# Optimization experiments

Hardware: AMD Instinct MI355X
Metric: run time of the kernel (lower is better)

The kernel has to match this reference:

```python
import jax, jax.numpy as jnp
import numpy as np

# PiGNNLayer(d_emb=128, n_heads=1, n_neighbors=30); N nodes, E = N*K edges, BSZ graphs
N, K, H, D = 16384, 30, 1, 128
E = N * K
DH = D // H  # d_head
BSZ = 1      # batch_idx is all zeros (see notes: gating broadcast requires bsz==1)


def setup_inputs() -> dict:
    key = jax.random.key(0)
    ks = jax.random.split(key, 16)

    def W(k, i, o):
        return jax.random.normal(k, (i, o), jnp.float32) / np.float32(np.sqrt(i))

    inp = {
        "h": jax.random.normal(ks[0], (N, D), jnp.float32),
        "e": jax.random.normal(ks[1], (E, D), jnp.float32),
        # att_mlp: Linear(3D,D) ReLU Linear(D,D) ReLU Linear(D,H)
        "aw1": W(ks[2], 3 * D, D), "ab1": jnp.zeros((D,), jnp.float32),
        "aw2": W(ks[3], D, D),     "ab2": jnp.zeros((D,), jnp.float32),
        "aw3": W(ks[4], D, H),     "ab3": jnp.zeros((H,), jnp.float32),
        # node_mlp: Linear(2D,D) GELU Linear(D,D) GELU Linear(D,D)
        "nw1": W(ks[5], 2 * D, D), "nb1": jnp.zeros((D,), jnp.float32),
        "nw2": W(ks[6], D, D),     "nb2": jnp.zeros((D,), jnp.float32),
        "nw3": W(ks[7], D, D),     "nb3": jnp.zeros((D,), jnp.float32),
        # to_h: Linear(D, D, bias=False)
        "thw": W(ks[8], H * D, D),
        # gate_mlp: Linear(D,D) ReLU Linear(D,D) ReLU Linear(D,D)
        "gw1": W(ks[9], D, D),  "gb1": jnp.zeros((D,), jnp.float32),
        "gw2": W(ks[10], D, D), "gb2": jnp.zeros((D,), jnp.float32),
        "gw3": W(ks[11], D, D), "gb3": jnp.zeros((D,), jnp.float32),
        # edge_idx[0] = source node i repeated K times (required by '(i j)' reshape)
        "edge_idx": jnp.stack([
            jnp.repeat(jnp.arange(N, dtype=jnp.int32), K),
            jax.random.randint(ks[12], (E,), 0, N, dtype=jnp.int32),
        ]),
        "batch_idx": jnp.zeros((N,), jnp.int32),
    }
    return inp


def reference(h, e, aw1, ab1, aw2, ab2, aw3, ab3,
              nw1, nb1, nw2, nb2, nw3, nb3, thw,
              gw1, gb1, gw2, gb2, gw3, gb3,
              edge_idx, batch_idx):
    src, dst = edge_idx[0], edge_idx[1]
    hi, hj = h[src], h[dst]                       # [E, D] gathers
    cat3 = jnp.concatenate([hi, e, hj], axis=-1)  # [E, 3D]
    cat2 = jnp.concatenate([e, hj], axis=-1)      # [E, 2D]

    # attention logits per head, grouped (i j) -> [H, N, K]
    w = jax.nn.relu(cat3 @ aw1 + ab1)
    w = jax.nn.relu(w @ aw2 + ab2)
    w = (w @ aw3 + ab3)                           # [E, H]
    w = jnp.transpose(w.reshape(N, K, H), (2, 0, 1)) / jnp.sqrt(jnp.float32(DH))
    att = jax.nn.softmax(w, axis=-1)              # softmax over neighbors j

    # values per edge (exact GELU, matching torch nn.GELU default)
    v = jax.nn.gelu(cat2 @ nw1 + nb1, approximate=False)
    v = jax.nn.gelu(v @ nw2 + nb2, approximate=False)
    v = (v @ nw3 + nb3).reshape(N, K, D)          # [N, K, D]

    hh = jnp.einsum('hij,ijd->ihd', att, v).reshape(N, H * D)  # 'h i d -> i (h d)'
    hh = hh @ thw                                 # to_h (no bias)

    # scatter_mean over batch (segment-sum form of the dense-mask trick)
    csum = jax.ops.segment_sum(hh, batch_idx, num_segments=BSZ)
    cnt = jax.ops.segment_sum(jnp.ones((N, 1), hh.dtype), batch_idx, num_segments=BSZ)
    c = csum / cnt                                # [BSZ, D]

    g = jax.nn.relu(c @ gw1 + gb1)
    g = jax.nn.relu(g @ gw2 + gb2)
    g = jax.nn.sigmoid(g @ gw3 + gb3)             # [BSZ, D]
    return hh * g[batch_idx]                      # per-node gate gather
```

## Files before the change

### kernel.cpp

```cpp
#include <hip/hip_runtime.h>
#include <math.h>

#define NN 16384
#define KNB 30
#define NE (NN*KNB)

typedef __attribute__((ext_vector_type(8))) __bf16 bf16x8;
typedef __attribute__((ext_vector_type(4))) float f32x4;
typedef unsigned short ushortT;
typedef __attribute__((ext_vector_type(8))) unsigned short ushort8v;

#define SWZ(r) (((r)&7)<<4)

__device__ __forceinline__ ushortT f2bf(float x){
  __bf16 b = (__bf16)x;
  union { __bf16 b; ushortT u; } v; v.b = b; return v.u;
}
__device__ __forceinline__ float bf2f(ushortT u){
  union { unsigned int u32; float f; } v; v.u32 = ((unsigned int)u) << 16;
  return v.f;
}
__device__ __forceinline__ float bf2f_lo(unsigned int w){
  union { unsigned int u32; float f; } v; v.u32 = w << 16; return v.f;
}
__device__ __forceinline__ float bf2f_hi(unsigned int w){
  union { unsigned int u32; float f; } v; v.u32 = w & 0xffff0000u; return v.f;
}
__device__ __forceinline__ float gelu_f(float x){
  float ax = fabsf(x) * 0.7071067811865476f;
  float t = 1.0f / (1.0f + 0.47047f * ax);
  float poly = t*(0.3480242f + t*(-0.0958798f + t*0.7478556f));
  float er = 1.0f - poly * __expf(-ax*ax);
  er = copysignf(er, x);
  return 0.5f * x * (1.0f + er);
}

__global__ void prep_kernel(const float* __restrict__ h,
                            const float* __restrict__ aw1, const float* __restrict__ nw1,
                            const float* __restrict__ aw2, const float* __restrict__ nw2,
                            const float* __restrict__ nw3, const float* __restrict__ nb3,
                            const float* __restrict__ thw,
                            const float* __restrict__ ab1, const float* __restrict__ nb1,
                            const float* __restrict__ ab2, const float* __restrict__ nb2,
                            ushortT* __restrict__ WF1, ushortT* __restrict__ WF2,
                            float* __restrict__ bias1, float* __restrict__ bias2,
                            float* __restrict__ U, ushortT* __restrict__ WVhP,
                            float* __restrict__ M, float* __restrict__ c3)
{
  __shared__ float sbuf[8*128];
  int tid = threadIdx.x;
  int b = blockIdx.x;

  if (b < 2048) {
    size_t n0 = (size_t)b * 8;
    if (tid < 256) {
      int r = tid >> 5, c = (tid & 31) * 4;
      *(float4*)&sbuf[r*128 + c] = *(const float4*)(h + (n0 + r)*128 + c);
    }
    __syncthreads();
    int d = tid & 127, seg = tid >> 7;
    const float* wbase = (seg == 0) ? (aw1 + d)
                       : (seg == 1) ? (aw1 + 256*128 + d)
                                    : (nw1 + 128*128 + d);
    float s[8] = {0.f,0.f,0.f,0.f,0.f,0.f,0.f,0.f};
    for (int c = 0; c < 128; ++c) {
      float w = wbase[(size_t)c*128];
      #pragma unroll
      for (int r = 0; r < 8; ++r) s[r] += sbuf[r*128 + c] * w;
    }
    if (seg == 0) {
      #pragma unroll
      for (int r = 0; r < 8; ++r) U[(n0 + r)*128 + d] = s[r];
    } else {
      int g = seg - 1;
      int idx = ((g*4 + (d >> 5))*16 + (d & 15))*2 + ((d >> 4) & 1);
      #pragma unroll
      for (int r = 0; r < 8; ++r) WVhP[(n0 + r)*256 + idx] = f2bf(s[r]);
    }
    return;
  }
  if (b < 2107) {
    if (tid >= 256) return;
    int u = (b - 2048) * 256 + tid;
    if (u < 8192) {
      int lane = u & 63, tile = u >> 6;
      int half = tile >> 6, nt = (tile >> 3) & 7, kt = tile & 7;
      int mrow = lane & 15, krow = lane >> 4;
      int n = half*128 + nt*16 + mrow, k0 = kt*32 + krow*8;
      ushort8v o;
      #pragma unroll
      for (int j = 0; j < 8; ++j) {
        int k = k0 + j;
        float v = (half == 0) ? aw1[(128 + k)*128 + n] : nw1[k*128 + (n - 128)];
        o[j] = f2bf(v);
      }
      *(ushort8v*)(WF1 + (size_t)u*8) = o;
      return;
    }
    u -= 8192;
    if (u < 4096) {
      int lane = u & 63, tile = u >> 6;
      int half = tile >> 5, nt = (tile >> 2) & 7, kt = tile & 3;
      int mrow = lane & 15, krow = lane >> 4;
      int n = half*128 + nt*16 + mrow, k0 = kt*32 + krow*8;
      ushort8v o;
      #pragma unroll
      for (int j = 0; j < 8; ++j) {
        int k = k0 + j;
        float v = (half == 0) ? aw2[k*128 + n] : nw2[k*128 + (n - 128)];
        o[j] = f2bf(v);
      }
      *(ushort8v*)(WF2 + (size_t)u*8) = o;
      return;
    }
    u -= 4096;
    if (u < 256) { bias1[u] = (u < 128) ? ab1[u] : nb1[u - 128]; return; }
    u -= 256;
    if (u < 256) { bias2[u] = (u < 128) ? ab2[u] : nb2[u - 128]; return; }
    return;
  }
  {
    if (tid >= 128) return;
    int bb = b - 2107;
    int d = tid;
    sbuf[d] = (bb < 128) ? nw3[bb*128 + d] : nb3[d];
    __syncthreads();
    float s = 0.f;
    for (int n = 0; n < 128; ++n) s += sbuf[n] * thw[n*128 + d];
    if (bb < 128) M[bb*128 + d] = s;
    else c3[d] = s;
  }
}

__global__ __launch_bounds__(512, 8) void edge_kernel(
    const float* __restrict__ e,
    const int* __restrict__ edge_idx,
    const ushortT* __restrict__ WVhP,
    const ushortT* __restrict__ WF1, const ushortT* __restrict__ WF2,
    const float* __restrict__ bias1, const float* __restrict__ bias2,
    const float* __restrict__ aw3, const float* __restrict__ ab3,
    float* __restrict__ hh)
{
  extern __shared__ char smem[];
  char*  Xb   = smem;
  float* lgp  = (float*)(smem + 16384);
  float* Ubs  = (float*)(smem + 16896);

  const int tid  = threadIdx.x;
  const int lane = tid & 63;
  const int wid  = tid >> 6;
  const int node = blockIdx.x;
  const long e0 = (long)node * KNB;

  const int mrow = lane & 15, krow = lane >> 4;
  const int wr = wid >> 2;
  const int wq = wid & 3;
  const int row = wr*16 + mrow;

  float uval = 0.f;
  if (tid < 128) uval = hh[(size_t)node*128 + tid];

  int dstr[4];
  #pragma unroll
  for (int rr = 0; rr < 4; ++rr) {
    int orow = wr*16 + krow*4 + rr;
    dstr[rr] = (orow < KNB) ? edge_idx[NE + e0 + orow] : -1;
  }

  {
    int r = tid >> 4, c8 = tid & 15;
    ushort8v u = {0,0,0,0,0,0,0,0};
    if (r < KNB) {
      const float* src = e + ((size_t)(e0 + r))*128 + c8*8;
      float4 v0 = *(const float4*)src;
      float4 v1 = *(const float4*)(src + 4);
      u[0]=f2bf(v0.x); u[1]=f2bf(v0.y); u[2]=f2bf(v0.z); u[3]=f2bf(v0.w);
      u[4]=f2bf(v1.x); u[5]=f2bf(v1.y); u[6]=f2bf(v1.z); u[7]=f2bf(v1.w);
    }
    *(ushort8v*)(Xb + r*512 + ((c8*16) ^ SWZ(r))) = u;
  }

  unsigned int wva[4], wvn[4];
  #pragma unroll
  for (int rr = 0; rr < 4; ++rr) {
    wva[rr] = 0u; wvn[rr] = 0u;
    if (dstr[rr] >= 0) {
      const unsigned int* base = (const unsigned int*)(WVhP + (size_t)dstr[rr]*256);
      wva[rr] = base[wq*16 + mrow];
      wvn[rr] = base[64 + wq*16 + mrow];
    }
  }
  if (tid < 128) Ubs[tid] = uval;
  asm volatile("s_waitcnt lgkmcnt(0)" ::: "memory");
  __builtin_amdgcn_s_barrier();

  const float b1a0 = bias1[wq*32 + mrow],        b1a1 = bias1[wq*32 + 16 + mrow];
  const float b1n0 = bias1[128 + wq*32 + mrow],  b1n1 = bias1[128 + wq*32 + 16 + mrow];
  const float b2a0 = bias2[wq*32 + mrow],        b2a1 = bias2[wq*32 + 16 + mrow];
  const float b2n0 = bias2[128 + wq*32 + mrow],  b2n1 = bias2[128 + wq*32 + 16 + mrow];
  const float aw3c0 = aw3[wq*32 + mrow]      * 0.08838834764831845f;
  const float aw3c1 = aw3[wq*32 + 16 + mrow] * 0.08838834764831845f;

  f32x4 acc[4];
  #pragma unroll
  for (int nt = 0; nt < 4; ++nt) acc[nt] = (f32x4){0.f,0.f,0.f,0.f};

  #pragma unroll
  for (int kt = 0; kt < 4; ++kt) {
    bf16x8 a = *(const bf16x8*)(Xb + row*512 + ((kt*64 + krow*16) ^ SWZ(row)));
    const ushortT* Ba = WF1 + ((size_t)(wq*2)*8 + kt)*512 + lane*8;
    const ushortT* Bn = WF1 + ((size_t)(8 + wq*2)*8 + kt)*512 + lane*8;
    acc[0] = __builtin_amdgcn_mfma_f32_16x16x32_bf16(a, *(const bf16x8*)Ba, acc[0], 0, 0, 0);
    acc[1] = __builtin_amdgcn_mfma_f32_16x16x32_bf16(a, *(const bf16x8*)(Ba + 8*512), acc[1], 0, 0, 0);
    acc[2] = __builtin_amdgcn_mfma_f32_16x16x32_bf16(a, *(const bf16x8*)Bn, acc[2], 0, 0, 0);
    acc[3] = __builtin_amdgcn_mfma_f32_16x16x32_bf16(a, *(const bf16x8*)(Bn + 8*512), acc[3], 0, 0, 0);
  }
  __syncthreads();

  {
    const float b1u0 = b1a0 + Ubs[wq*32 + mrow];
    const float b1u1 = b1a1 + Ubs[wq*32 + 16 + mrow];
    #pragma unroll
    for (int rr = 0; rr < 4; ++rr) {
      int orow = wr*16 + krow*4 + rr;
      char* xrow = Xb + orow*512;
      int sw = SWZ(orow);
      int ca0 = 2*(wq*32 + mrow),        ca1 = 2*(wq*32 + 16 + mrow);
      float x0 = fmaxf(acc[0][rr] + b1u0 + bf2f_lo(wva[rr]), 0.f);
      float x1 = fmaxf(acc[1][rr] + b1u1 + bf2f_hi(wva[rr]), 0.f);
      *(ushortT*)(xrow + (ca0 ^ sw)) = f2bf(x0);
      *(ushortT*)(xrow + (ca1 ^ sw)) = f2bf(x1);
      float y0 = gelu_f(acc[2][rr] + b1n0 + bf2f_lo(wvn[rr]));
      float y1 = gelu_f(acc[3][rr] + b1n1 + bf2f_hi(wvn[rr]));
      *(ushortT*)(xrow + ((256 + ca0) ^ sw)) = f2bf(y0);
      *(ushortT*)(xrow + ((256 + ca1) ^ sw)) = f2bf(y1);
    }
  }
  __syncthreads();

  #pragma unroll
  for (int nt = 0; nt < 4; ++nt) acc[nt] = (f32x4){0.f,0.f,0.f,0.f};
  #pragma unroll
  for (int kt = 0; kt < 4; ++kt) {
    bf16x8 a0 = *(const bf16x8*)(Xb + row*512 + ((kt*64 + krow*16) ^ SWZ(row)));
    bf16x8 a1 = *(const bf16x8*)(Xb + row*512 + ((256 + kt*64 + krow*16) ^ SWZ(row)));
    const ushortT* Ba = WF2 + ((size_t)(wq*2)*4 + kt)*512 + lane*8;
    const ushortT* Bn = WF2 + ((size_t)(8 + wq*2)*4 + kt)*512 + lane*8;
    acc[0] = __builtin_amdgcn_mfma_f32_16x16x32_bf16(a0, *(const bf16x8*)Ba, acc[0], 0, 0, 0);
    acc[1] = __builtin_amdgcn_mfma_f32_16x16x32_bf16(a0, *(const bf16x8*)(Ba + 4*512), acc[1], 0, 0, 0);
    acc[2] = __builtin_amdgcn_mfma_f32_16x16x32_bf16(a1, *(const bf16x8*)Bn, acc[2], 0, 0, 0);
    acc[3] = __builtin_amdgcn_mfma_f32_16x16x32_bf16(a1, *(const bf16x8*)(Bn + 4*512), acc[3], 0, 0, 0);
  }
  __syncthreads();
  {
    #pragma unroll
    for (int rr = 0; rr < 4; ++rr) {
      int orow = wr*16 + krow*4 + rr;
      int sw = SWZ(orow);
      float lsum = fmaxf(acc[0][rr] + b2a0, 0.f) * aw3c0
                 + fmaxf(acc[1][rr] + b2a1, 0.f) * aw3c1;
      lsum += __shfl_xor(lsum, 1);
      lsum += __shfl_xor(lsum, 2);
      lsum += __shfl_xor(lsum, 4);
      lsum += __shfl_xor(lsum, 8);
      if (mrow == 0) lgp[wq*32 + orow] = lsum;
      char* xrow = Xb + orow*512;
      float y0 = gelu_f(acc[2][rr] + b2n0);
      float y1 = gelu_f(acc[3][rr] + b2n1);
      *(ushortT*)(xrow + ((2*(wq*32 + mrow)) ^ sw)) = f2bf(y0);
      *(ushortT*)(xrow + ((2*(wq*32 + 16 + mrow)) ^ sw)) = f2bf(y1);
    }
  }
  __syncthreads();

  {
    float x = -INFINITY;
    if (lane < KNB)
      x = lgp[lane] + lgp[32 + lane] + lgp[64 + lane] + lgp[96 + lane];
    float m = x;
    #pragma unroll
    for (int off = 16; off >= 1; off >>= 1) m = fmaxf(m, __shfl_xor(m, off));
    float p = (lane < KNB) ? __expf(x - m) : 0.f;
    float ssum = p;
    #pragma unroll
    for (int off = 16; off >= 1; off >>= 1) ssum += __shfl_xor(ssum, off);
    float attv = p / ssum;

    int pr = lane & 7, ks = lane >> 3;
    int col0 = wid*16 + pr*2;
    float s0 = 0.f, s1 = 0.f;
    #pragma unroll
    for (int j = 0; j < 4; ++j) {
      int k2 = ks + 8*j;
      float a = __shfl(attv, k2);
      unsigned int w = *(const unsigned int*)(Xb + k2*512 + ((2*col0) ^ SWZ(k2)));
      s0 += a * bf2f_lo(w);
      s1 += a * bf2f_hi(w);
    }
    s0 += __shfl_xor(s0, 8);  s1 += __shfl_xor(s1, 8);
    s0 += __shfl_xor(s0, 16); s1 += __shfl_xor(s1, 16);
    s0 += __shfl_xor(s0, 32); s1 += __shfl_xor(s1, 32);
    if (lane < 8) {
      float2 o; o.x = s0; o.y = s1;
      *(float2*)(hh + (size_t)node*128 + col0) = o;
    }
  }
}

__global__ void reduce1_kernel(const float* __restrict__ hh, float* __restrict__ p2) {
  int b = blockIdx.x, tid = threadIdx.x;
  int d = tid & 127, half = tid >> 7;
  float s = 0.f;
  const float* base = hh + (size_t)(b*64 + half*32)*128 + d;
  #pragma unroll 4
  for (int i = 0; i < 32; ++i) s += base[(size_t)i*128];
  __shared__ float ps[256];
  ps[tid] = s; __syncthreads();
  if (tid < 128) p2[b*128 + tid] = ps[tid] + ps[tid + 128];
}

__global__ void gate_kernel(const float* __restrict__ p2,
                            const float* __restrict__ M, const float* __restrict__ c3,
                            const float* __restrict__ gw1, const float* __restrict__ gb1,
                            const float* __restrict__ gw2, const float* __restrict__ gb2,
                            const float* __restrict__ gw3, const float* __restrict__ gb3,
                            float* __restrict__ gout) {
  int tid = threadIdx.x;
  int d = tid & 127, half = tid >> 7;
  float s = 0.f;
  for (int i = 0; i < 128; ++i) s += p2[(half*128 + i)*128 + d];
  __shared__ float ps[256];
  __shared__ float cv[128], cv2[128], y1[128], y2[128];
  ps[tid] = s; __syncthreads();
  if (tid < 128) cv[tid] = (ps[tid] + ps[tid+128]) * (1.f / (float)NN);
  __syncthreads();
  if (tid < 128) {
    float a = c3[tid];
    for (int c = 0; c < 128; ++c) a += cv[c] * M[c*128 + tid];
    cv2[tid] = a;
  }
  __syncthreads();
  if (tid < 128) {
    float a = gb1[tid];
    for (int c = 0; c < 128; ++c) a += cv2[c] * gw1[c*128 + tid];
    y1[tid] = fmaxf(a, 0.f);
  }
  __syncthreads();
  if (tid < 128) {
    float a = gb2[tid];
    for (int c = 0; c < 128; ++c) a += y1[c] * gw2[c*128 + tid];
    y2[tid] = fmaxf(a, 0.f);
  }
  __syncthreads();
  if (tid < 128) {
    float a = gb3[tid];
    for (int c = 0; c < 128; ++c) a += y2[c] * gw3[c*128 + tid];
    gout[tid] = 1.f / (1.f + __expf(-a));
  }
}

__global__ void toh_scale_kernel(float* __restrict__ hh, const float* __restrict__ M,
                                 const float* __restrict__ c3,
                                 const float* __restrict__ gv)
{
  __shared__ float hs[16][128];
  int tid = threadIdx.x;
  size_t n0 = (size_t)blockIdx.x * 16;
  {
    int r = tid >> 4, c = (tid & 15) * 8;
    const float* src = hh + (n0 + r)*128 + c;
    *(float4*)&hs[r][c]     = *(const float4*)src;
    *(float4*)&hs[r][c + 4] = *(const float4*)(src + 4);
  }
  __syncthreads();
  int d = tid & 127, gq = tid >> 7;
  float s[8] = {0.f,0.f,0.f,0.f,0.f,0.f,0.f,0.f};
  for (int c = 0; c < 128; ++c) {
    float w = M[c*128 + d];
    #pragma unroll
    for (int r = 0; r < 8; ++r) s[r] += hs[gq*8 + r][c] * w;
  }
  float gd = gv[d];
  float cd = c3[d];
  #pragma unroll
  for (int r = 0; r < 8; ++r) hh[(n0 + gq*8 + r)*128 + d] = (s[r] + cd) * gd;
}

extern "C" void kernel_launch(void* const* d_in, const int* in_sizes, int n_in,
                              void* d_out, int out_size, void* d_ws, size_t ws_size,
                              hipStream_t stream) {
  const float* h   = (const float*)d_in[0];
  const float* e   = (const float*)d_in[1];
  const float* aw1 = (const float*)d_in[2];
  const float* ab1 = (const float*)d_in[3];
  const float* aw2 = (const float*)d_in[4];
  const float* ab2 = (const float*)d_in[5];
  const float* aw3 = (const float*)d_in[6];
  const float* ab3 = (const float*)d_in[7];
  const float* nw1 = (const float*)d_in[8];
  const float* nb1 = (const float*)d_in[9];
  const float* nw2 = (const float*)d_in[10];
  const float* nb2 = (const float*)d_in[11];
  const float* nw3 = (const float*)d_in[12];
  const float* nb3 = (const float*)d_in[13];
  const float* thw = (const float*)d_in[14];
  const float* gw1 = (const float*)d_in[15];
  const float* gb1 = (const float*)d_in[16];
  const float* gw2 = (const float*)d_in[17];
  const float* gb2 = (const float*)d_in[18];
  const float* gw3 = (const float*)d_in[19];
  const float* gb3 = (const float*)d_in[20];
  const int* edge_idx = (const int*)d_in[21];

  char* ws = (char*)d_ws;
  ushortT* WF1 = (ushortT*)(ws + 0);
  ushortT* WF2 = (ushortT*)(ws + 131072);
  float* bias1 = (float*)(ws + 196608);
  float* bias2 = (float*)(ws + 197632);
  float* p2    = (float*)(ws + 198656);
  float* gout  = (float*)(ws + 329728);
  float* Mw    = (float*)(ws + 330240);
  float* c3w   = (float*)(ws + 395776);
  ushortT* WVhP= (ushortT*)(ws + 396288);
  float* hh    = (float*)d_out;

  prep_kernel<<<2236, 384, 0, stream>>>(h, aw1, nw1, aw2, nw2, nw3, nb3, thw,
                                        ab1, nb1, ab2, nb2,
                                        WF1, WF2, bias1, bias2,
                                        hh, WVhP, Mw, c3w);

  const int SMEM = 17408;
  hipFuncSetAttribute((const void*)edge_kernel,
                      hipFuncAttributeMaxDynamicSharedMemorySize, SMEM);
  edge_kernel<<<NN, 512, SMEM, stream>>>(e, edge_idx, WVhP, WF1, WF2,
                                         bias1, bias2, aw3, ab3, hh);

  reduce1_kernel<<<256, 256, 0, stream>>>(hh, p2);
  gate_kernel<<<1, 256, 0, stream>>>(p2, Mw, c3w, gw1, gb1, gw2, gb2, gw3, gb3, gout);
  toh_scale_kernel<<<NN/16, 256, 0, stream>>>(hh, Mw, c3w, gout);
}
```

Baseline: 327.0 us.

## Halve edge-kernel block to 4 waves, each computing two M tiles to reuse B

The edge kernel now runs 256 threads (4 waves) per node instead of 512. Each wave computes both 16-row M tiles, so every B fragment loaded from global weights feeds two MFMAs instead of one. Weight tiles are re-laid so each lane owns an adjacent column pair, which lets the epilogue write packed 32-bit bf16 pairs to LDS. This reduces redundant weight loads and LDS store count, at the cost of more registers per thread and less per-block parallelism.

```diff
diff --git a/kernel.cpp b/kernel.cpp
--- a/kernel.cpp
+++ b/kernel.cpp
@@ -72,10 +72,9 @@
       #pragma unroll
       for (int r = 0; r < 8; ++r) U[(n0 + r)*128 + d] = s[r];
     } else {
-      int g = seg - 1;
-      int idx = ((g*4 + (d >> 5))*16 + (d & 15))*2 + ((d >> 4) & 1);
-      #pragma unroll
-      for (int r = 0; r < 8; ++r) WVhP[(n0 + r)*256 + idx] = f2bf(s[r]);
+      int off = (seg - 1) * 128;
+      #pragma unroll
+      for (int r = 0; r < 8; ++r) WVhP[(n0 + r)*256 + off + d] = f2bf(s[r]);
     }
     return;
   }
@@ -86,7 +85,8 @@
       int lane = u & 63, tile = u >> 6;
       int half = tile >> 6, nt = (tile >> 3) & 7, kt = tile & 7;
       int mrow = lane & 15, krow = lane >> 4;
-      int n = half*128 + nt*16 + mrow, k0 = kt*32 + krow*8;
+      int g = nt >> 1, p = nt & 1;
+      int n = half*128 + g*32 + 2*mrow + p, k0 = kt*32 + krow*8;
       ushort8v o;
       #pragma unroll
       for (int j = 0; j < 8; ++j) {
@@ -102,7 +102,8 @@
       int lane = u & 63, tile = u >> 6;
       int half = tile >> 5, nt = (tile >> 2) & 7, kt = tile & 3;
       int mrow = lane & 15, krow = lane >> 4;
-      int n = half*128 + nt*16 + mrow, k0 = kt*32 + krow*8;
+      int g = nt >> 1, p = nt & 1;
+      int n = half*128 + g*32 + 2*mrow + p, k0 = kt*32 + krow*8;
       ushort8v o;
       #pragma unroll
       for (int j = 0; j < 8; ++j) {
@@ -132,7 +133,7 @@
   }
 }
 
-__global__ __launch_bounds__(512, 8) void edge_kernel(
+__global__ __launch_bounds__(256, 7) void edge_kernel(
     const float* __restrict__ e,
     const int* __restrict__ edge_idx,
     const ushortT* __restrict__ WVhP,
@@ -148,27 +149,19 @@
 
   const int tid  = threadIdx.x;
   const int lane = tid & 63;
-  const int wid  = tid >> 6;
+  const int wq   = tid >> 6;
   const int node = blockIdx.x;
   const long e0 = (long)node * KNB;
 
   const int mrow = lane & 15, krow = lane >> 4;
-  const int wr = wid >> 2;
-  const int wq = wid & 3;
-  const int row = wr*16 + mrow;
 
   float uval = 0.f;
   if (tid < 128) uval = hh[(size_t)node*128 + tid];
 
-  int dstr[4];
-  #pragma unroll
-  for (int rr = 0; rr < 4; ++rr) {
-    int orow = wr*16 + krow*4 + rr;
-    dstr[rr] = (orow < KNB) ? edge_idx[NE + e0 + orow] : -1;
-  }
-
-  {
-    int r = tid >> 4, c8 = tid & 15;
+  #pragma unroll
+  for (int it = 0; it < 2; ++it) {
+    int idx = it*256 + tid;
+    int r = idx >> 4, c8 = idx & 15;
     ushort8v u = {0,0,0,0,0,0,0,0};
     if (r < KNB) {
       const float* src = e + ((size_t)(e0 + r))*128 + c8*8;
@@ -180,96 +173,130 @@
     *(ushort8v*)(Xb + r*512 + ((c8*16) ^ SWZ(r))) = u;
   }
 
-  unsigned int wva[4], wvn[4];
-  #pragma unroll
-  for (int rr = 0; rr < 4; ++rr) {
-    wva[rr] = 0u; wvn[rr] = 0u;
-    if (dstr[rr] >= 0) {
-      const unsigned int* base = (const unsigned int*)(WVhP + (size_t)dstr[rr]*256);
-      wva[rr] = base[wq*16 + mrow];
-      wvn[rr] = base[64 + wq*16 + mrow];
+  unsigned int wva[8], wvn[8];
+  #pragma unroll
+  for (int g = 0; g < 8; ++g) {
+    int row_ = (g >> 2)*16 + krow*4 + (g & 3);
+    wva[g] = 0u; wvn[g] = 0u;
+    if (row_ < KNB) {
+      int dst = edge_idx[NE + e0 + row_];
+      const unsigned int* base = (const unsigned int*)(WVhP + (size_t)dst*256);
+      wva[g] = base[wq*16 + mrow];
+      wvn[g] = base[64 + wq*16 + mrow];
     }
   }
   if (tid < 128) Ubs[tid] = uval;
   asm volatile("s_waitcnt lgkmcnt(0)" ::: "memory");
   __builtin_amdgcn_s_barrier();
 
-  const float b1a0 = bias1[wq*32 + mrow],        b1a1 = bias1[wq*32 + 16 + mrow];
-  const float b1n0 = bias1[128 + wq*32 + mrow],  b1n1 = bias1[128 + wq*32 + 16 + mrow];
-  const float b2a0 = bias2[wq*32 + mrow],        b2a1 = bias2[wq*32 + 16 + mrow];
-  const float b2n0 = bias2[128 + wq*32 + mrow],  b2n1 = bias2[128 + wq*32 + 16 + mrow];
-  const float aw3c0 = aw3[wq*32 + mrow]      * 0.08838834764831845f;
-  const float aw3c1 = aw3[wq*32 + 16 + mrow] * 0.08838834764831845f;
-
-  f32x4 acc[4];
-  #pragma unroll
-  for (int nt = 0; nt < 4; ++nt) acc[nt] = (f32x4){0.f,0.f,0.f,0.f};
+  const int ca = wq*32 + 2*mrow;
+  const int cn = 128 + ca;
+  const float b1a0 = bias1[ca],  b1a1 = bias1[ca+1];
+  const float b1n0 = bias1[cn],  b1n1 = bias1[cn+1];
+  const float b2a0 = bias2[ca],  b2a1 = bias2[ca+1];
+  const float b2n0 = bias2[cn],  b2n1 = bias2[cn+1];
+  const float aw3c0 = aw3[ca]   * 0.08838834764831845f;
+  const float aw3c1 = aw3[ca+1] * 0.08838834764831845f;
+  const int pairb = 4*(wq*16 + mrow);
+
+  f32x4 acc[2][4];
+  #pragma unroll
+  for (int mt = 0; mt < 2; ++mt)
+    #pragma unroll
+    for (int nt = 0; nt < 4; ++nt) acc[mt][nt] = (f32x4){0.f,0.f,0.f,0.f};
 
   #pragma unroll
   for (int kt = 0; kt < 4; ++kt) {
-    bf16x8 a = *(const bf16x8*)(Xb + row*512 + ((kt*64 + krow*16) ^ SWZ(row)));
+    int koff = kt*64 + krow*16;
+    bf16x8 a0 = *(const bf16x8*)(Xb + mrow*512 + (koff ^ SWZ(mrow)));
+    bf16x8 a1 = *(const bf16x8*)(Xb + (16 + mrow)*512 + (koff ^ SWZ(16 + mrow)));
     const ushortT* Ba = WF1 + ((size_t)(wq*2)*8 + kt)*512 + lane*8;
     const ushortT* Bn = WF1 + ((size_t)(8 + wq*2)*8 + kt)*512 + lane*8;
-    acc[0] = __builtin_amdgcn_mfma_f32_16x16x32_bf16(a, *(const bf16x8*)Ba, acc[0], 0, 0, 0);
-    acc[1] = __builtin_amdgcn_mfma_f32_16x16x32_bf16(a, *(const bf16x8*)(Ba + 8*512), acc[1], 0, 0, 0);
-    acc[2] = __builtin_amdgcn_mfma_f32_16x16x32_bf16(a, *(const bf16x8*)Bn, acc[2], 0, 0, 0);
-    acc[3] = __builtin_amdgcn_mfma_f32_16x16x32_bf16(a, *(const bf16x8*)(Bn + 8*512), acc[3], 0, 0, 0);
+    bf16x8 ba0 = *(const bf16x8*)Ba;
+    bf16x8 ba1 = *(const bf16x8*)(Ba + 8*512);
+    bf16x8 bn0 = *(const bf16x8*)Bn;
+    bf16x8 bn1 = *(const bf16x8*)(Bn + 8*512);
+    acc[0][0] = __builtin_amdgcn_mfma_f32_16x16x32_bf16(a0, ba0, acc[0][0], 0, 0, 0);
+    acc[0][1] = __builtin_amdgcn_mfma_f32_16x16x32_bf16(a0, ba1, acc[0][1], 0, 0, 0);
+    acc[0][2] = __builtin_amdgcn_mfma_f32_16x16x32_bf16(a0, bn0, acc[0][2], 0, 0, 0);
+    acc[0][3] = __builtin_amdgcn_mfma_f32_16x16x32_bf16(a0, bn1, acc[0][3], 0, 0, 0);
+    acc[1][0] = __builtin_amdgcn_mfma_f32_16x16x32_bf16(a1, ba0, acc[1][0], 0, 0, 0);
+    acc[1][1] = __builtin_amdgcn_mfma_f32_16x16x32_bf16(a1, ba1, acc[1][1], 0, 0, 0);
+    acc[1][2] = __builtin_amdgcn_mfma_f32_16x16x32_bf16(a1, bn0, acc[1][2], 0, 0, 0);
+    acc[1][3] = __builtin_amdgcn_mfma_f32_16x16x32_bf16(a1, bn1, acc[1][3], 0, 0, 0);
   }
   __syncthreads();
 
   {
-    const float b1u0 = b1a0 + Ubs[wq*32 + mrow];
-    const float b1u1 = b1a1 + Ubs[wq*32 + 16 + mrow];
-    #pragma unroll
-    for (int rr = 0; rr < 4; ++rr) {
-      int orow = wr*16 + krow*4 + rr;
-      char* xrow = Xb + orow*512;
-      int sw = SWZ(orow);
-      int ca0 = 2*(wq*32 + mrow),        ca1 = 2*(wq*32 + 16 + mrow);
-      float x0 = fmaxf(acc[0][rr] + b1u0 + bf2f_lo(wva[rr]), 0.f);
-      float x1 = fmaxf(acc[1][rr] + b1u1 + bf2f_hi(wva[rr]), 0.f);
-      *(ushortT*)(xrow + (ca0 ^ sw)) = f2bf(x0);
-      *(ushortT*)(xrow + (ca1 ^ sw)) = f2bf(x1);
-      float y0 = gelu_f(acc[2][rr] + b1n0 + bf2f_lo(wvn[rr]));
-      float y1 = gelu_f(acc[3][rr] + b1n1 + bf2f_hi(wvn[rr]));
-      *(ushortT*)(xrow + ((256 + ca0) ^ sw)) = f2bf(y0);
-      *(ushortT*)(xrow + ((256 + ca1) ^ sw)) = f2bf(y1);
-    }
-  }
-  __syncthreads();
-
-  #pragma unroll
-  for (int nt = 0; nt < 4; ++nt) acc[nt] = (f32x4){0.f,0.f,0.f,0.f};
+    const float b1u0 = b1a0 + Ubs[ca];
+    const float b1u1 = b1a1 + Ubs[ca+1];
+    #pragma unroll
+    for (int mt = 0; mt < 2; ++mt)
+      #pragma unroll
+      for (int rr = 0; rr < 4; ++rr) {
+        int row_ = mt*16 + krow*4 + rr;
+        int g = mt*4 + rr;
+        char* xrow = Xb + row_*512;
+        int sw = SWZ(row_);
+        float x0 = fmaxf(acc[mt][0][rr] + b1u0 + bf2f_lo(wva[g]), 0.f);
+        float x1 = fmaxf(acc[mt][1][rr] + b1u1 + bf2f_hi(wva[g]), 0.f);
+        unsigned int pa = (unsigned int)f2bf(x0) | ((unsigned int)f2bf(x1) << 16);
+        *(unsigned int*)(xrow + (pairb ^ sw)) = pa;
+        float y0 = gelu_f(acc[mt][2][rr] + b1n0 + bf2f_lo(wvn[g]));
+        float y1 = gelu_f(acc[mt][3][rr] + b1n1 + bf2f_hi(wvn[g]));
+        unsigned int pn = (unsigned int)f2bf(y0) | ((unsigned int)f2bf(y1) << 16);
+        *(unsigned int*)(xrow + ((256 + pairb) ^ sw)) = pn;
+      }
+  }
+  __syncthreads();
+
+  #pragma unroll
+  for (int mt = 0; mt < 2; ++mt)
+    #pragma unroll
+    for (int nt = 0; nt < 4; ++nt) acc[mt][nt] = (f32x4){0.f,0.f,0.f,0.f};
   #pragma unroll
   for (int kt = 0; kt < 4; ++kt) {
-    bf16x8 a0 = *(const bf16x8*)(Xb + row*512 + ((kt*64 + krow*16) ^ SWZ(row)));
-    bf16x8 a1 = *(const bf16x8*)(Xb + row*512 + ((256 + kt*64 + krow*16) ^ SWZ(row)));
+    int koff = kt*64 + krow*16;
+    bf16x8 aw0 = *(const bf16x8*)(Xb + mrow*512 + (koff ^ SWZ(mrow)));
+    bf16x8 aw1v = *(const bf16x8*)(Xb + (16 + mrow)*512 + (koff ^ SWZ(16 + mrow)));
+    bf16x8 av0 = *(const bf16x8*)(Xb + mrow*512 + ((256 + koff) ^ SWZ(mrow)));
+    bf16x8 av1 = *(const bf16x8*)(Xb + (16 + mrow)*512 + ((256 + koff) ^ SWZ(16 + mrow)));
     const ushortT* Ba = WF2 + ((size_t)(wq*2)*4 + kt)*512 + lane*8;
     const ushortT* Bn = WF2 + ((size_t)(8 + wq*2)*4 + kt)*512 + lane*8;
-    acc[0] = __builtin_amdgcn_mfma_f32_16x16x32_bf16(a0, *(const bf16x8*)Ba, acc[0], 0, 0, 0);
-    acc[1] = __builtin_amdgcn_mfma_f32_16x16x32_bf16(a0, *(const bf16x8*)(Ba + 4*512), acc[1], 0, 0, 0);
-    acc[2] = __builtin_amdgcn_mfma_f32_16x16x32_bf16(a1, *(const bf16x8*)Bn, acc[2], 0, 0, 0);
-    acc[3] = __builtin_amdgcn_mfma_f32_16x16x32_bf16(a1, *(const bf16x8*)(Bn + 4*512), acc[3], 0, 0, 0);
-  }
-  __syncthreads();
+    bf16x8 ba0 = *(const bf16x8*)Ba;
+    bf16x8 ba1 = *(const bf16x8*)(Ba + 4*512);
+    bf16x8 bn0 = *(const bf16x8*)Bn;
+    bf16x8 bn1 = *(const bf16x8*)(Bn + 4*512);
+    acc[0][0] = __builtin_amdgcn_mfma_f32_16x16x32_bf16(aw0, ba0, acc[0][0], 0, 0, 0);
+    acc[0][1] = __builtin_amdgcn_mfma_f32_16x16x32_bf16(aw0, ba1, acc[0][1], 0, 0, 0);
+    acc[0][2] = __builtin_amdgcn_mfma_f32_16x16x32_bf16(av0, bn0, acc[0][2], 0, 0, 0);
+    acc[0][3] = __builtin_amdgcn_mfma_f32_16x16x32_bf16(av0, bn1, acc[0][3], 0, 0, 0);
+    acc[1][0] = __builtin_amdgcn_mfma_f32_16x16x32_bf16(aw1v, ba0, acc[1][0], 0, 0, 0);
+    acc[1][1] = __builtin_amdgcn_mfma_f32_16x16x32_bf16(aw1v, ba1, acc[1][1], 0, 0, 0);
+    acc[1][2] = __builtin_amdgcn_mfma_f32_16x16x32_bf16(av1, bn0, acc[1][2], 0, 0, 0);
+    acc[1][3] = __builtin_amdgcn_mfma_f32_16x16x32_bf16(av1, bn1, acc[1][3], 0, 0, 0);
+  }
+  __syncthreads();
+
   {
     #pragma unroll
-    for (int rr = 0; rr < 4; ++rr) {
-      int orow = wr*16 + krow*4 + rr;
-      int sw = SWZ(orow);
-      float lsum = fmaxf(acc[0][rr] + b2a0, 0.f) * aw3c0
-                 + fmaxf(acc[1][rr] + b2a1, 0.f) * aw3c1;
-      lsum += __shfl_xor(lsum, 1);
-      lsum += __shfl_xor(lsum, 2);
-      lsum += __shfl_xor(lsum, 4);
-      lsum += __shfl_xor(lsum, 8);
-      if (mrow == 0) lgp[wq*32 + orow] = lsum;
-      char* xrow = Xb + orow*512;
-      float y0 = gelu_f(acc[2][rr] + b2n0);
-      float y1 = gelu_f(acc[3][rr] + b2n1);
-      *(ushortT*)(xrow + ((2*(wq*32 + mrow)) ^ sw)) = f2bf(y0);
-      *(ushortT*)(xrow + ((2*(wq*32 + 16 + mrow)) ^ sw)) = f2bf(y1);
-    }
+    for (int mt = 0; mt < 2; ++mt)
+      #pragma unroll
+      for (int rr = 0; rr < 4; ++rr) {
+        int row_ = mt*16 + krow*4 + rr;
+        int sw = SWZ(row_);
+        float lsum = fmaxf(acc[mt][0][rr] + b2a0, 0.f) * aw3c0
+                   + fmaxf(acc[mt][1][rr] + b2a1, 0.f) * aw3c1;
+        lsum += __shfl_xor(lsum, 1);
+        lsum += __shfl_xor(lsum, 2);
+        lsum += __shfl_xor(lsum, 4);
+        lsum += __shfl_xor(lsum, 8);
+        if (mrow == 0) lgp[wq*32 + row_] = lsum;
+        float y0 = gelu_f(acc[mt][2][rr] + b2n0);
+        float y1 = gelu_f(acc[mt][3][rr] + b2n1);
+        unsigned int pn = (unsigned int)f2bf(y0) | ((unsigned int)f2bf(y1) << 16);
+        *(unsigned int*)(Xb + row_*512 + (pairb ^ sw)) = pn;
+      }
   }
   __syncthreads();
 
@@ -286,21 +313,21 @@
     for (int off = 16; off >= 1; off >>= 1) ssum += __shfl_xor(ssum, off);
     float attv = p / ssum;
 
-    int pr = lane & 7, ks = lane >> 3;
-    int col0 = wid*16 + pr*2;
+    int pr = lane & 15, ks = lane >> 4;
+    int col0 = wq*32 + pr*2;
+    int pb = 4*(wq*16 + pr);
     float s0 = 0.f, s1 = 0.f;
     #pragma unroll
-    for (int j = 0; j < 4; ++j) {
-      int k2 = ks + 8*j;
+    for (int j = 0; j < 8; ++j) {
+      int k2 = ks + 4*j;
       float a = __shfl(attv, k2);
-      unsigned int w = *(const unsigned int*)(Xb + k2*512 + ((2*col0) ^ SWZ(k2)));
+      unsigned int w = *(const unsigned int*)(Xb + k2*512 + (pb ^ SWZ(k2)));
       s0 += a * bf2f_lo(w);
       s1 += a * bf2f_hi(w);
     }
-    s0 += __shfl_xor(s0, 8);  s1 += __shfl_xor(s1, 8);
     s0 += __shfl_xor(s0, 16); s1 += __shfl_xor(s1, 16);
     s0 += __shfl_xor(s0, 32); s1 += __shfl_xor(s1, 32);
-    if (lane < 8) {
+    if (lane < 16) {
       float2 o; o.x = s0; o.y = s1;
       *(float2*)(hh + (size_t)node*128 + col0) = o;
     }
@@ -432,7 +459,7 @@
   const int SMEM = 17408;
   hipFuncSetAttribute((const void*)edge_kernel,
                       hipFuncAttributeMaxDynamicSharedMemorySize, SMEM);
-  edge_kernel<<<NN, 512, SMEM, stream>>>(e, edge_idx, WVhP, WF1, WF2,
+  edge_kernel<<<NN, 256, SMEM, stream>>>(e, edge_idx, WVhP, WF1, WF2,
                                          bias1, bias2, aw3, ab3, hh);
 
   reduce1_kernel<<<256, 256, 0, stream>>>(hh, p2);
```

Result: slower. 427.8 us (+30.8%).
